# Performance work log

Measured on AMD Instinct MI355X. Metric: run time of the kernel, lower is better.

Reference implementation:

```python
import jax, jax.numpy as jnp
import numpy as np

N_NODES = 50000
NEG_SLOPE = 0.2  # PyG GATConv default leaky_relu slope


def setup_inputs() -> dict:
    key = jax.random.key(0)
    ks = jax.random.split(key, 12)
    N, E, D_IN, H = N_NODES, 1200000, 128, 64
    sd_in = 1.0 / np.sqrt(D_IN)
    sd_h = 1.0 / np.sqrt(H)
    return {
        "x": jax.random.normal(ks[0], (N, D_IN), jnp.float32),
        "src": jax.random.randint(ks[1], (E,), 0, N, jnp.int32),
        "dst": jax.random.randint(ks[2], (E,), 0, N, jnp.int32),
        "W1_src": jax.random.normal(ks[3], (D_IN, H), jnp.float32) * sd_in,
        "W1_dst": jax.random.normal(ks[4], (D_IN, H), jnp.float32) * sd_in,
        "a1_src": jax.random.normal(ks[5], (H,), jnp.float32) * sd_h,
        "a1_dst": jax.random.normal(ks[6], (H,), jnp.float32) * sd_h,
        "b1": jnp.zeros((H,), jnp.float32),
        "W2_src": jax.random.normal(ks[7], (H, H), jnp.float32) * sd_h,
        "W2_dst": jax.random.normal(ks[8], (H, H), jnp.float32) * sd_h,
        "a2_src": jax.random.normal(ks[9], (H,), jnp.float32) * sd_h,
        "a2_dst": jax.random.normal(ks[10], (H,), jnp.float32) * sd_h,
        "b2": jnp.zeros((H,), jnp.float32),
    }


def _gat_layer(x, src, dst, W_src, W_dst, att_src, att_dst, bias):
    N = x.shape[0]
    h_src = x @ W_src            # [N, H] transformed source features
    h_dst = x @ W_dst            # [N, H] transformed destination features
    alpha_src = h_src @ att_src  # [N]
    alpha_dst = h_dst @ att_dst  # [N]
    # edge-wise attention logits (gather), edge j -> i: e = lrelu(a_src[j] + a_dst[i])
    e = jax.nn.leaky_relu(alpha_src[src] + alpha_dst[dst], NEG_SLOPE)  # [E]
    # segment softmax over incoming edges of each destination node
    m = jax.ops.segment_max(e, dst, num_segments=N)          # [N]
    ex = jnp.exp(e - m[dst])                                  # [E]
    denom = jax.ops.segment_sum(ex, dst, num_segments=N)     # [N]
    alpha = ex / denom[dst]                                   # [E]
    # weighted scatter-add aggregation
    msgs = h_src[src] * alpha[:, None]                        # [E, H]
    out = jax.ops.segment_sum(msgs, dst, num_segments=N)     # [N, H]
    return out + bias


def reference(x, src, dst, W1_src, W1_dst, a1_src, a1_dst, b1,
              W2_src, W2_dst, a2_src, a2_dst, b2):
    h = jnp.tanh(_gat_layer(x, src, dst, W1_src, W1_dst, a1_src, a1_dst, b1))
    h = jnp.tanh(_gat_layer(h, src, dst, W2_src, W2_dst, a2_src, a2_dst, b2))
    return h
```

## Files before the change

kernel.cpp:

```cpp
#include <hip/hip_runtime.h>
#include <hip/hip_bf16.h>

#define NEG_SLOPE 0.2f
#define EPB 4096

typedef __attribute__((ext_vector_type(8))) short short8v;
typedef __attribute__((ext_vector_type(4))) float f32x4;

__device__ inline float blo(unsigned u) { return __uint_as_float(u << 16); }
__device__ inline float bhi(unsigned u) { return __uint_as_float(u & 0xffff0000u); }
__device__ inline unsigned short bf16bits(float f) {
    __hip_bfloat16 b = __float2bfloat16(f);
    return *(unsigned short*)&b;
}
__device__ inline unsigned pack2bf(float e, float o) {
    return ((unsigned)bf16bits(o) << 16) | (unsigned)bf16bits(e);
}

__global__ void init_counts(int* __restrict__ bucket_cnt) {
    bucket_cnt[threadIdx.x] = 0;
}

__global__ __launch_bounds__(256) void bucket_hist(const int* __restrict__ dst,
                                                   int* __restrict__ bucket_cnt, int E) {
    __shared__ int lh[256];
    int tid = threadIdx.x;
    lh[tid] = 0;
    __syncthreads();
    for (int e = blockIdx.x * 256 + tid; e < E; e += gridDim.x * 256)
        atomicAdd(&lh[dst[e] >> 8], 1);
    __syncthreads();
    if (lh[tid]) atomicAdd(&bucket_cnt[tid], lh[tid]);
}

__global__ __launch_bounds__(256) void bucket_scan(const int* __restrict__ bucket_cnt,
                                                   int* __restrict__ bucket_base,
                                                   int* __restrict__ bucket_cursor, int NB) {
    __shared__ int tmp[256];
    int tid = threadIdx.x;
    int v = (tid < NB) ? bucket_cnt[tid] : 0;
    tmp[tid] = v;
    __syncthreads();
    for (int off = 1; off < 256; off <<= 1) {
        int t = (tid >= off) ? tmp[tid - off] : 0;
        __syncthreads();
        tmp[tid] += t;
        __syncthreads();
    }
    int excl = tmp[tid] - v;
    bucket_base[tid] = excl;
    bucket_cursor[tid] = excl;
    if (tid == 255) bucket_base[256] = tmp[255];
}

__global__ __launch_bounds__(256) void bucket_scatter(const int* __restrict__ src,
                                                      const int* __restrict__ dst,
                                                      int* __restrict__ bucket_cursor,
                                                      unsigned* __restrict__ ebuf, int E) {
    __shared__ int lhist[256];
    __shared__ int lbase[256];
    int tid = threadIdx.x;
    lhist[tid] = 0;
    __syncthreads();
    int base = blockIdx.x * EPB;
    int bkt[16], rank[16];
    unsigned pack[16];
    #pragma unroll
    for (int i = 0; i < 16; ++i) {
        int e = base + i * 256 + tid;
        bkt[i] = -1;
        if (e < E) {
            int d = dst[e], s = src[e];
            bkt[i]  = d >> 8;
            pack[i] = ((unsigned)(d & 255) << 16) | (unsigned)s;
            rank[i] = atomicAdd(&lhist[bkt[i]], 1);
        }
    }
    __syncthreads();
    int cnt = lhist[tid];
    if (cnt) lbase[tid] = atomicAdd(&bucket_cursor[tid], cnt);
    __syncthreads();
    #pragma unroll
    for (int i = 0; i < 16; ++i)
        if (bkt[i] >= 0) ebuf[lbase[bkt[i]] + rank[i]] = pack[i];
}

__global__ __launch_bounds__(256) void bucket_build(const unsigned* __restrict__ ebuf,
                                                    const int* __restrict__ bucket_base,
                                                    int* __restrict__ row_ptr,
                                                    int* __restrict__ csr_src,
                                                    int N, int E) {
    __shared__ int deg[256];
    __shared__ int cur[256];
    __shared__ int tmp[256];
    int b = blockIdx.x, tid = threadIdx.x;
    int ebase = bucket_base[b], eend = bucket_base[b + 1];
    deg[tid] = 0;
    __syncthreads();
    for (int e = ebase + tid; e < eend; e += 256)
        atomicAdd(&deg[ebuf[e] >> 16], 1);
    __syncthreads();
    int v = deg[tid];
    tmp[tid] = v;
    __syncthreads();
    for (int off = 1; off < 256; off <<= 1) {
        int t = (tid >= off) ? tmp[tid - off] : 0;
        __syncthreads();
        tmp[tid] += t;
        __syncthreads();
    }
    int excl = tmp[tid] - v;
    int node = b * 256 + tid;
    if (node < N) row_ptr[node] = ebase + excl;
    if (b == 0 && tid == 0) row_ptr[N] = E;
    cur[tid] = excl;
    __syncthreads();
    for (int e = ebase + tid; e < eend; e += 256) {
        unsigned pk = ebuf[e];
        int r = atomicAdd(&cur[pk >> 16], 1);
        csr_src[ebase + r] = (int)(pk & 0xFFFFu);
    }
}

template <int K, bool INBF16>
__global__ __launch_bounds__(256) void node_transform_mfma(
    const void* __restrict__ x_,
    const float* __restrict__ W_src,
    const float* __restrict__ a_src,
    const float* __restrict__ W_dst,
    const float* __restrict__ a_dst,
    unsigned* __restrict__ hb_out,
    float* __restrict__ alpha_src,
    float* __restrict__ alpha_dst,
    int N) {
    constexpr int PAD = K + 8;
    __shared__ unsigned short sBt[80 * PAD];
    __shared__ unsigned short sX[64 * PAD];

    int tid = threadIdx.x;
    for (int i = tid; i < 64 * K; i += 256) {
        int k = i >> 6, j = i & 63;
        sBt[j * PAD + k] = bf16bits(W_src[i]);
    }
    for (int i = tid; i < 2 * K; i += 256) {
        int which = (i >= K) ? 1 : 0;
        int k = i - which * K;
        const float* Wr = (which ? W_dst : W_src) + k * 64;
        const float* av = which ? a_dst : a_src;
        float s = 0.f;
        #pragma unroll
        for (int j = 0; j < 64; ++j) s += Wr[j] * av[j];
        sBt[(64 + which) * PAD + k] = bf16bits(s);
    }
    for (int i = tid; i < 14 * K; i += 256) {
        int j = 66 + i / K, k = i % K;
        sBt[j * PAD + k] = 0;
    }
    if constexpr (!INBF16) {
        const float* xb = (const float*)x_;
        for (int idx = tid; idx < 64 * K / 4; idx += 256) {
            int row = (idx * 4) / K, col = (idx * 4) % K;
            int g = blockIdx.x * 64 + row;
            const float4 f = *(const float4*)(xb + (size_t)((g < N) ? g : N - 1) * K + col);
            unsigned short* d = &sX[row * PAD + col];
            d[0] = bf16bits(f.x); d[1] = bf16bits(f.y);
            d[2] = bf16bits(f.z); d[3] = bf16bits(f.w);
        }
    } else {
        const unsigned short* xb = (const unsigned short*)x_;
        for (int idx = tid; idx < 64 * K / 8; idx += 256) {
            int row = (idx * 8) / K, col = (idx * 8) % K;
            int g = blockIdx.x * 64 + row;
            short8v v = *(const short8v*)(xb + (size_t)((g < N) ? g : N - 1) * K + col);
            *(short8v*)&sX[row * PAD + col] = v;
        }
    }
    __syncthreads();

    int wid = tid >> 6, l = tid & 63;
    int rowbase = blockIdx.x * 64 + wid * 16;
    int jcol = l & 15;

    f32x4 acc[5];
    #pragma unroll
    for (int t = 0; t < 5; ++t) acc[t] = (f32x4){0.f, 0.f, 0.f, 0.f};

    const unsigned short* xrow = &sX[(wid * 16 + (l & 15)) * PAD + (l >> 4) * 8];
    #pragma unroll
    for (int kt = 0; kt < K / 32; ++kt) {
        short8v a = *(const short8v*)(xrow + kt * 32);
        int kbase = kt * 32 + (l >> 4) * 8;
        #pragma unroll
        for (int t = 0; t < 5; ++t) {
            short8v b = *(const short8v*)&sBt[(t * 16 + jcol) * PAD + kbase];
            acc[t] = __builtin_amdgcn_mfma_f32_16x16x32_bf16(a, b, acc[t], 0, 0, 0);
        }
    }

    int rbase = rowbase + (l >> 4) * 4;
    #pragma unroll
    for (int t = 0; t < 4; ++t) {
        #pragma unroll
        for (int r = 0; r < 4; ++r) {
            float v = acc[t][r];
            float w = __shfl_xor(v, 1);
            int row = rbase + r;
            if (!(l & 1) && row < N)
                hb_out[(size_t)row * 32 + t * 8 + (jcol >> 1)] = pack2bf(v, w);
        }
    }
    #pragma unroll
    for (int r = 0; r < 4; ++r) {
        int row = rbase + r;
        if (row < N) {
            if (jcol == 0) alpha_src[row] = acc[4][r];
            if (jcol == 1) alpha_dst[row] = acc[4][r];
        }
    }
}

template <bool OUTBF16>
__global__ __launch_bounds__(256) void aggregate(
    const int* __restrict__ row_ptr, const int* __restrict__ csr_src,
    const float* __restrict__ alpha_src, const float* __restrict__ alpha_dst,
    const unsigned* __restrict__ hb,
    const float* __restrict__ bias,
    void* __restrict__ out_,
    int N) {
    int wid = threadIdx.x >> 6, lane = threadIdx.x & 63;
    int node = blockIdx.x * 4 + wid;
    if (node >= N) return;

    int beg = row_ptr[node], end = row_ptr[node + 1];
    float adst = alpha_dst[node];
    int half = lane >> 5, sub = lane & 31;

    float dL = 0.f;
    float aA[4] = {0.f, 0.f, 0.f, 0.f};
    float aB[4] = {0.f, 0.f, 0.f, 0.f};

    for (int c = beg; c < end; c += 64) {
        int cnt = end - c;
        cnt = (cnt < 64) ? cnt : 64;

        int s = 0;
        float p = 0.f;
        if (lane < cnt) {
            s = csr_src[c + lane];
            float t = alpha_src[s] + adst;
            t = (t > 0.f) ? t : NEG_SLOPE * t;
            p = __expf(fminf(t, 60.f));
            dL += p;
        }

        for (int j = 0; j < cnt; j += 16) {
            int   sv[8];
            float pv[8];
            unsigned uv[8];
            #pragma unroll
            for (int i = 0; i < 8; ++i) {
                int e = j + 2 * i + half;
                sv[i] = __shfl(s, e);
                pv[i] = __shfl(p, e);
            }
            #pragma unroll
            for (int i = 0; i < 8; ++i)
                uv[i] = hb[(size_t)sv[i] * 32 + sub];
            #pragma unroll
            for (int i = 0; i < 8; ++i) {
                aA[i & 3] = fmaf(pv[i], blo(uv[i]), aA[i & 3]);
                aB[i & 3] = fmaf(pv[i], bhi(uv[i]), aB[i & 3]);
            }
        }
    }
    float denom = dL;
    #pragma unroll
    for (int off = 32; off; off >>= 1) denom += __shfl_xor(denom, off);

    float accA = (aA[0] + aA[1]) + (aA[2] + aA[3]);
    float accB = (aB[0] + aB[1]) + (aB[2] + aB[3]);
    accA += __shfl_xor(accA, 32);
    accB += __shfl_xor(accB, 32);
    int srcl = lane >> 1;
    float vA = __shfl(accA, srcl);
    float vB = __shfl(accB, srcl);
    float val = (lane & 1) ? vB : vA;
    float r = (denom > 0.f) ? (val / denom) : 0.f;
    float fv = tanhf(r + bias[lane]);

    if constexpr (OUTBF16) {
        float fw = __shfl_xor(fv, 1);
        if (!(lane & 1))
            ((unsigned*)out_)[(size_t)node * 32 + (lane >> 1)] = pack2bf(fv, fw);
    } else {
        ((float*)out_)[(size_t)node * 64 + lane] = fv;
    }
}

extern "C" void kernel_launch(void* const* d_in, const int* in_sizes, int n_in,
                              void* d_out, int out_size, void* d_ws, size_t ws_size,
                              hipStream_t stream) {
    const float* x      = (const float*)d_in[0];
    const int*   src    = (const int*)  d_in[1];
    const int*   dst    = (const int*)  d_in[2];
    const float* W1_src = (const float*)d_in[3];
    const float* W1_dst = (const float*)d_in[4];
    const float* a1_src = (const float*)d_in[5];
    const float* a1_dst = (const float*)d_in[6];
    const float* b1     = (const float*)d_in[7];
    const float* W2_src = (const float*)d_in[8];
    const float* W2_dst = (const float*)d_in[9];
    const float* a2_src = (const float*)d_in[10];
    const float* a2_dst = (const float*)d_in[11];
    const float* b2     = (const float*)d_in[12];
    float* out = (float*)d_out;

    const int N = in_sizes[0] / 128;
    const int E = in_sizes[1];
    const int NB = (N + 255) / 256;

    char* ws = (char*)d_ws;
    size_t off = 0;
    auto alloc = [&](size_t bytes) {
        void* p = ws + off;
        off += (bytes + 255) & ~(size_t)255;
        return p;
    };
    unsigned* hbuf   = (unsigned*)alloc((size_t)N * 32 * 4);
    unsigned* h1buf  = (unsigned*)alloc((size_t)N * 32 * 4);
    float* alpha_src = (float*)alloc((size_t)N * 4);
    float* alpha_dst = (float*)alloc((size_t)N * 4);
    int*   row_ptr   = (int*)  alloc((size_t)(N + 1) * 4);
    int*   csr_src   = (int*)  alloc((size_t)E * 4);
    int*   bucket_cnt    = (int*)alloc(256 * 4);
    int*   bucket_base   = (int*)alloc(257 * 4);
    int*   bucket_cursor = (int*)alloc(256 * 4);
    unsigned* ebuf = (unsigned*)alloc((size_t)E * 4);
    (void)ws_size;

    const int eb3   = (E + EPB - 1) / EPB;
    const int aggb  = (N + 3) / 4;
    const int mfb   = (N + 63) / 64;

    init_counts<<<1, 256, 0, stream>>>(bucket_cnt);
    bucket_hist<<<256, 256, 0, stream>>>(dst, bucket_cnt, E);
    bucket_scan<<<1, 256, 0, stream>>>(bucket_cnt, bucket_base, bucket_cursor, NB);
    bucket_scatter<<<eb3, 256, 0, stream>>>(src, dst, bucket_cursor, ebuf, E);
    bucket_build<<<NB, 256, 0, stream>>>(ebuf, bucket_base, row_ptr, csr_src, N, E);

    node_transform_mfma<128, false><<<mfb, 256, 0, stream>>>(
        x, W1_src, a1_src, W1_dst, a1_dst, hbuf, alpha_src, alpha_dst, N);
    aggregate<true><<<aggb, 256, 0, stream>>>(row_ptr, csr_src, alpha_src, alpha_dst,
                                              hbuf, b1, h1buf, N);

    node_transform_mfma<64, true><<<mfb, 256, 0, stream>>>(
        h1buf, W2_src, a2_src, W2_dst, a2_dst, hbuf, alpha_src, alpha_dst, N);
    aggregate<false><<<aggb, 256, 0, stream>>>(row_ptr, csr_src, alpha_src, alpha_dst,
                                               hbuf, b2, out, N);
}
```

Before: 148.5 us.

## Fuse layer-1 transform with histogram and layer-1 aggregation with layer-2 transform

Layer 1's node transform and the destination histogram now run in one launch, with extra blocks writing per-block partial histograms. Those partials are summed in the scan, so the init kernel and global atomics go away. Layer 1's aggregation is fused with layer 2's MFMA transform: each block aggregates 64 nodes into shared memory and transforms them directly, skipping the global write and re-read of h1. This cuts launches and intermediate memory traffic, but the fused aggregate now runs 16 nodes serially per wave and restages the weights in every block, which may lower parallelism.

```diff
diff --git a/kernel.cpp b/kernel.cpp
--- a/kernel.cpp
+++ b/kernel.cpp
@@ -3,6 +3,7 @@
 
 #define NEG_SLOPE 0.2f
 #define EPB 4096
+#define NHB 64
 
 typedef __attribute__((ext_vector_type(8))) short short8v;
 typedef __attribute__((ext_vector_type(4))) float f32x4;
@@ -17,28 +18,128 @@
     return ((unsigned)bf16bits(o) << 16) | (unsigned)bf16bits(e);
 }
 
-__global__ void init_counts(int* __restrict__ bucket_cnt) {
-    bucket_cnt[threadIdx.x] = 0;
-}
-
-__global__ __launch_bounds__(256) void bucket_hist(const int* __restrict__ dst,
-                                                   int* __restrict__ bucket_cnt, int E) {
+template <int K>
+__device__ inline void stage_sBt(unsigned short* sBt,
+                                 const float* __restrict__ W_src,
+                                 const float* __restrict__ a_src,
+                                 const float* __restrict__ W_dst,
+                                 const float* __restrict__ a_dst, int tid) {
+    constexpr int PAD = K + 8;
+    for (int i = tid; i < 64 * K; i += 256) {
+        int k = i >> 6, j = i & 63;
+        sBt[j * PAD + k] = bf16bits(W_src[i]);
+    }
+    for (int i = tid; i < 2 * K; i += 256) {
+        int which = (i >= K) ? 1 : 0;
+        int k = i - which * K;
+        const float* Wr = (which ? W_dst : W_src) + k * 64;
+        const float* av = which ? a_dst : a_src;
+        float s = 0.f;
+        #pragma unroll
+        for (int j = 0; j < 64; ++j) s += Wr[j] * av[j];
+        sBt[(64 + which) * PAD + k] = bf16bits(s);
+    }
+    for (int i = tid; i < 14 * K; i += 256) {
+        int j = 66 + i / K, k = i % K;
+        sBt[j * PAD + k] = 0;
+    }
+}
+
+template <int K>
+__device__ inline void nt_mfma_body(const unsigned short* sBt,
+                                    const unsigned short* sX,
+                                    int rowblockbase,
+                                    unsigned* __restrict__ hb_out,
+                                    float* __restrict__ alpha_src,
+                                    float* __restrict__ alpha_dst,
+                                    int N, int tid) {
+    constexpr int PAD = K + 8;
+    int wid = tid >> 6, l = tid & 63;
+    int jcol = l & 15;
+
+    f32x4 acc[5];
+    #pragma unroll
+    for (int t = 0; t < 5; ++t) acc[t] = (f32x4){0.f, 0.f, 0.f, 0.f};
+
+    const unsigned short* xrow = &sX[(wid * 16 + (l & 15)) * PAD + (l >> 4) * 8];
+    #pragma unroll
+    for (int kt = 0; kt < K / 32; ++kt) {
+        short8v a = *(const short8v*)(xrow + kt * 32);
+        int kbase = kt * 32 + (l >> 4) * 8;
+        #pragma unroll
+        for (int t = 0; t < 5; ++t) {
+            short8v b = *(const short8v*)&sBt[(t * 16 + jcol) * PAD + kbase];
+            acc[t] = __builtin_amdgcn_mfma_f32_16x16x32_bf16(a, b, acc[t], 0, 0, 0);
+        }
+    }
+
+    int rbase = rowblockbase + wid * 16 + (l >> 4) * 4;
+    #pragma unroll
+    for (int t = 0; t < 4; ++t) {
+        #pragma unroll
+        for (int r = 0; r < 4; ++r) {
+            float v = acc[t][r];
+            float w = __shfl_xor(v, 1);
+            int row = rbase + r;
+            if (!(l & 1) && row < N)
+                hb_out[(size_t)row * 32 + t * 8 + (jcol >> 1)] = pack2bf(v, w);
+        }
+    }
+    #pragma unroll
+    for (int r = 0; r < 4; ++r) {
+        int row = rbase + r;
+        if (row < N) {
+            if (jcol == 0) alpha_src[row] = acc[4][r];
+            if (jcol == 1) alpha_dst[row] = acc[4][r];
+        }
+    }
+}
+
+__global__ __launch_bounds__(256) void fused_nt1_hist(
+    const float* __restrict__ x,
+    const float* __restrict__ W_src, const float* __restrict__ a_src,
+    const float* __restrict__ W_dst, const float* __restrict__ a_dst,
+    unsigned* __restrict__ hb_out, float* __restrict__ alpha_src,
+    float* __restrict__ alpha_dst, int N,
+    const int* __restrict__ dst, int* __restrict__ partials, int E, int ntb) {
+    constexpr int K = 128, PAD = K + 8;
+    __shared__ unsigned short sBt[80 * PAD];
+    __shared__ unsigned short sX[64 * PAD];
     __shared__ int lh[256];
     int tid = threadIdx.x;
-    lh[tid] = 0;
-    __syncthreads();
-    for (int e = blockIdx.x * 256 + tid; e < E; e += gridDim.x * 256)
-        atomicAdd(&lh[dst[e] >> 8], 1);
-    __syncthreads();
-    if (lh[tid]) atomicAdd(&bucket_cnt[tid], lh[tid]);
-}
-
-__global__ __launch_bounds__(256) void bucket_scan(const int* __restrict__ bucket_cnt,
+
+    if ((int)blockIdx.x >= ntb) {
+        int bh = blockIdx.x - ntb;
+        lh[tid] = 0;
+        __syncthreads();
+        for (int e = bh * 256 + tid; e < E; e += NHB * 256)
+            atomicAdd(&lh[dst[e] >> 8], 1);
+        __syncthreads();
+        partials[bh * 256 + tid] = lh[tid];
+        return;
+    }
+
+    stage_sBt<K>(sBt, W_src, a_src, W_dst, a_dst, tid);
+    for (int idx = tid; idx < 64 * K / 4; idx += 256) {
+        int row = (idx * 4) / K, col = (idx * 4) % K;
+        int g = blockIdx.x * 64 + row;
+        const float4 f = *(const float4*)(x + (size_t)((g < N) ? g : N - 1) * K + col);
+        unsigned short* d = &sX[row * PAD + col];
+        d[0] = bf16bits(f.x); d[1] = bf16bits(f.y);
+        d[2] = bf16bits(f.z); d[3] = bf16bits(f.w);
+    }
+    __syncthreads();
+    nt_mfma_body<K>(sBt, sX, blockIdx.x * 64, hb_out, alpha_src, alpha_dst, N, tid);
+}
+
+__global__ __launch_bounds__(256) void bucket_scan(const int* __restrict__ partials,
                                                    int* __restrict__ bucket_base,
-                                                   int* __restrict__ bucket_cursor, int NB) {
+                                                   int* __restrict__ bucket_cursor) {
     __shared__ int tmp[256];
     int tid = threadIdx.x;
-    int v = (tid < NB) ? bucket_cnt[tid] : 0;
+    int v = 0;
+    #pragma unroll 8
+    for (int b = 0; b < NHB; ++b) v += partials[b * 256 + tid];
     tmp[tid] = v;
     __syncthreads();
     for (int off = 1; off < 256; off <<= 1) {
@@ -122,115 +223,12 @@
     }
 }
 
-template <int K, bool INBF16>
-__global__ __launch_bounds__(256) void node_transform_mfma(
-    const void* __restrict__ x_,
-    const float* __restrict__ W_src,
-    const float* __restrict__ a_src,
-    const float* __restrict__ W_dst,
-    const float* __restrict__ a_dst,
-    unsigned* __restrict__ hb_out,
-    float* __restrict__ alpha_src,
-    float* __restrict__ alpha_dst,
-    int N) {
-    constexpr int PAD = K + 8;
-    __shared__ unsigned short sBt[80 * PAD];
-    __shared__ unsigned short sX[64 * PAD];
-
-    int tid = threadIdx.x;
-    for (int i = tid; i < 64 * K; i += 256) {
-        int k = i >> 6, j = i & 63;
-        sBt[j * PAD + k] = bf16bits(W_src[i]);
-    }
-    for (int i = tid; i < 2 * K; i += 256) {
-        int which = (i >= K) ? 1 : 0;
-        int k = i - which * K;
-        const float* Wr = (which ? W_dst : W_src) + k * 64;
-        const float* av = which ? a_dst : a_src;
-        float s = 0.f;
-        #pragma unroll
-        for (int j = 0; j < 64; ++j) s += Wr[j] * av[j];
-        sBt[(64 + which) * PAD + k] = bf16bits(s);
-    }
-    for (int i = tid; i < 14 * K; i += 256) {
-        int j = 66 + i / K, k = i % K;
-        sBt[j * PAD + k] = 0;
-    }
-    if constexpr (!INBF16) {
-        const float* xb = (const float*)x_;
-        for (int idx = tid; idx < 64 * K / 4; idx += 256) {
-            int row = (idx * 4) / K, col = (idx * 4) % K;
-            int g = blockIdx.x * 64 + row;
-            const float4 f = *(const float4*)(xb + (size_t)((g < N) ? g : N - 1) * K + col);
-            unsigned short* d = &sX[row * PAD + col];
-            d[0] = bf16bits(f.x); d[1] = bf16bits(f.y);
-            d[2] = bf16bits(f.z); d[3] = bf16bits(f.w);
-        }
-    } else {
-        const unsigned short* xb = (const unsigned short*)x_;
-        for (int idx = tid; idx < 64 * K / 8; idx += 256) {
-            int row = (idx * 8) / K, col = (idx * 8) % K;
-            int g = blockIdx.x * 64 + row;
-            short8v v = *(const short8v*)(xb + (size_t)((g < N) ? g : N - 1) * K + col);
-            *(short8v*)&sX[row * PAD + col] = v;
-        }
-    }
-    __syncthreads();
-
-    int wid = tid >> 6, l = tid & 63;
-    int rowbase = blockIdx.x * 64 + wid * 16;
-    int jcol = l & 15;
-
-    f32x4 acc[5];
-    #pragma unroll
-    for (int t = 0; t < 5; ++t) acc[t] = (f32x4){0.f, 0.f, 0.f, 0.f};
-
-    const unsigned short* xrow = &sX[(wid * 16 + (l & 15)) * PAD + (l >> 4) * 8];
-    #pragma unroll
-    for (int kt = 0; kt < K / 32; ++kt) {
-        short8v a = *(const short8v*)(xrow + kt * 32);
-        int kbase = kt * 32 + (l >> 4) * 8;
-        #pragma unroll
-        for (int t = 0; t < 5; ++t) {
-            short8v b = *(const short8v*)&sBt[(t * 16 + jcol) * PAD + kbase];
-            acc[t] = __builtin_amdgcn_mfma_f32_16x16x32_bf16(a, b, acc[t], 0, 0, 0);
-        }
-    }
-
-    int rbase = rowbase + (l >> 4) * 4;
-    #pragma unroll
-    for (int t = 0; t < 4; ++t) {
-        #pragma unroll
-        for (int r = 0; r < 4; ++r) {
-            float v = acc[t][r];
-            float w = __shfl_xor(v, 1);
-            int row = rbase + r;
-            if (!(l & 1) && row < N)
-                hb_out[(size_t)row * 32 + t * 8 + (jcol >> 1)] = pack2bf(v, w);
-        }
-    }
-    #pragma unroll
-    for (int r = 0; r < 4; ++r) {
-        int row = rbase + r;
-        if (row < N) {
-            if (jcol == 0) alpha_src[row] = acc[4][r];
-            if (jcol == 1) alpha_dst[row] = acc[4][r];
-        }
-    }
-}
-
-template <bool OUTBF16>
-__global__ __launch_bounds__(256) void aggregate(
-    const int* __restrict__ row_ptr, const int* __restrict__ csr_src,
-    const float* __restrict__ alpha_src, const float* __restrict__ alpha_dst,
-    const unsigned* __restrict__ hb,
-    const float* __restrict__ bias,
-    void* __restrict__ out_,
-    int N) {
-    int wid = threadIdx.x >> 6, lane = threadIdx.x & 63;
-    int node = blockIdx.x * 4 + wid;
-    if (node >= N) return;
-
+__device__ inline float agg_node(int node, const int* __restrict__ row_ptr,
+                                 const int* __restrict__ csr_src,
+                                 const float* __restrict__ alpha_src,
+                                 const float* __restrict__ alpha_dst,
+                                 const unsigned* __restrict__ hb,
+                                 float blane, int lane) {
     int beg = row_ptr[node], end = row_ptr[node + 1];
     float adst = alpha_dst[node];
     int half = lane >> 5, sub = lane & 31;
@@ -286,15 +284,52 @@
     float vB = __shfl(accB, srcl);
     float val = (lane & 1) ? vB : vA;
     float r = (denom > 0.f) ? (val / denom) : 0.f;
-    float fv = tanhf(r + bias[lane]);
-
-    if constexpr (OUTBF16) {
-        float fw = __shfl_xor(fv, 1);
-        if (!(lane & 1))
-            ((unsigned*)out_)[(size_t)node * 32 + (lane >> 1)] = pack2bf(fv, fw);
-    } else {
-        ((float*)out_)[(size_t)node * 64 + lane] = fv;
-    }
+    return tanhf(r + blane);
+}
+
+__global__ __launch_bounds__(256) void fused_agg_nt(
+    const int* __restrict__ row_ptr, const int* __restrict__ csr_src,
+    const float* __restrict__ alpha_src1, const float* __restrict__ alpha_dst1,
+    const unsigned* __restrict__ hb1,
+    const float* __restrict__ bias1,
+    const float* __restrict__ W_src, const float* __restrict__ a_src,
+    const float* __restrict__ W_dst, const float* __restrict__ a_dst,
+    unsigned* __restrict__ hb2, float* __restrict__ alpha_src2,
+    float* __restrict__ alpha_dst2, int N) {
+    constexpr int K = 64, PAD = K + 8;
+    __shared__ unsigned short sBt[80 * PAD];
+    __shared__ unsigned short sX[64 * PAD];
+    int tid = threadIdx.x;
+
+    stage_sBt<K>(sBt, W_src, a_src, W_dst, a_dst, tid);
+
+    int wid = tid >> 6, lane = tid & 63;
+    int blockbase = blockIdx.x * 64;
+    float blane = bias1[lane];
+
+    for (int i = 0; i < 16; ++i) {
+        int node = blockbase + wid * 16 + i;
+        float fv = 0.f;
+        if (node < N)
+            fv = agg_node(node, row_ptr, csr_src, alpha_src1, alpha_dst1, hb1,
+                          blane, lane);
+        sX[(wid * 16 + i) * PAD + lane] = bf16bits(fv);
+    }
+    __syncthreads();
+    nt_mfma_body<K>(sBt, sX, blockbase, hb2, alpha_src2, alpha_dst2, N, tid);
+}
+
+__global__ __launch_bounds__(256) void aggregate_out(
+    const int* __restrict__ row_ptr, const int* __restrict__ csr_src,
+    const float* __restrict__ alpha_src, const float* __restrict__ alpha_dst,
+    const unsigned* __restrict__ hb, const float* __restrict__ bias,
+    float* __restrict__ out, int N) {
+    int wid = threadIdx.x >> 6, lane = threadIdx.x & 63;
+    int node = blockIdx.x * 4 + wid;
+    if (node >= N) return;
+    float fv = agg_node(node, row_ptr, csr_src, alpha_src, alpha_dst, hb,
+                        bias[lane], lane);
+    out[(size_t)node * 64 + lane] = fv;
 }
 
 extern "C" void kernel_launch(void* const* d_in, const int* in_sizes, int n_in,
@@ -326,35 +361,33 @@
         off += (bytes + 255) & ~(size_t)255;
         return p;
     };
-    unsigned* hbuf   = (unsigned*)alloc((size_t)N * 32 * 4);
-    unsigned* h1buf  = (unsigned*)alloc((size_t)N * 32 * 4);
-    float* alpha_src = (float*)alloc((size_t)N * 4);
-    float* alpha_dst = (float*)alloc((size_t)N * 4);
-    int*   row_ptr   = (int*)  alloc((size_t)(N + 1) * 4);
-    int*   csr_src   = (int*)  alloc((size_t)E * 4);
-    int*   bucket_cnt    = (int*)alloc(256 * 4);
+    unsigned* hbuf1   = (unsigned*)alloc((size_t)N * 32 * 4);
+    unsigned* hbuf2   = (unsigned*)alloc((size_t)N * 32 * 4);
+    float* alpha_s1   = (float*)alloc((size_t)N * 4);
+    float* alpha_d1   = (float*)alloc((size_t)N * 4);
+    float* alpha_s2   = (float*)alloc((size_t)N * 4);
+    float* alpha_d2   = (float*)alloc((size_t)N * 4);
+    int*   row_ptr    = (int*)  alloc((size_t)(N + 1) * 4);
+    int*   csr_src    = (int*)  alloc((size_t)E * 4);
+    int*   partials   = (int*)  alloc(NHB * 256 * 4);
     int*   bucket_base   = (int*)alloc(257 * 4);
     int*   bucket_cursor = (int*)alloc(256 * 4);
-    unsigned* ebuf = (unsigned*)alloc((size_t)E * 4);
-    (void)ws_size;
-
-    const int eb3   = (E + EPB - 1) / EPB;
-    const int aggb  = (N + 3) / 4;
-    const int mfb   = (N + 63) / 64;
-
-    init_counts<<<1, 256, 0, stream>>>(bucket_cnt);
-    bucket_hist<<<256, 256, 0, stream>>>(dst, bucket_cnt, E);
-    bucket_scan<<<1, 256, 0, stream>>>(bucket_cnt, bucket_base, bucket_cursor, NB);
+    unsigned* ebuf    = (unsigned*)alloc((size_t)E * 4);
+    (void)ws_size; (void)NB;
+
+    const int eb3  = (E + EPB - 1) / EPB;
+    const int aggb = (N + 3) / 4;
+    const int ntb  = (N + 63) / 64;
+
+    fused_nt1_hist<<<ntb + NHB, 256, 0, stream>>>(
+        x, W1_src, a1_src, W1_dst, a1_dst, hbuf1, alpha_s1, alpha_d1, N,
+        dst, partials, E, ntb);
+    bucket_scan<<<1, 256, 0, stream>>>(partials, bucket_base, bucket_cursor);
     bucket_scatter<<<eb3, 256, 0, stream>>>(src, dst, bucket_cursor, ebuf, E);
     bucket_build<<<NB, 256, 0, stream>>>(ebuf, bucket_base, row_ptr, csr_src, N, E);
-
-    node_transform_mfma<128, false><<<mfb, 256, 0, stream>>>(
-        x, W1_src, a1_src, W1_dst, a1_dst, hbuf, alpha_src, alpha_dst, N);
-    aggregate<true><<<aggb, 256, 0, stream>>>(row_ptr, csr_src, alpha_src, alpha_dst,
-                                              hbuf, b1, h1buf, N);
-
-    node_transform_mfma<64, true><<<mfb, 256, 0, stream>>>(
-        h1buf, W2_src, a2_src, W2_dst, a2_dst, hbuf, alpha_src, alpha_dst, N);
-    aggregate<false><<<aggb, 256, 0, stream>>>(row_ptr, csr_src, alpha_src, alpha_dst,
-                                               hbuf, b2, out, N);
-}
+    fused_agg_nt<<<ntb, 256, 0, stream>>>(
+        row_ptr, csr_src, alpha_s1, alpha_d1, hbuf1, b1,
+        W2_src, a2_src, W2_dst, a2_dst, hbuf2, alpha_s2, alpha_d2, N);
+    aggregate_out<<<aggb, 256, 0, stream>>>(
+        row_ptr, csr_src, alpha_s2, alpha_d2, hbuf2, b2, out, N);
+}
```

After: 154.8 us. 1.04x slower.

## Precompute bf16 weight tiles once and load node features directly to registers

Applied to the files above, without the earlier changes.

The bf16 transposed weight matrices (plus the folded attention vectors) are now built once in a prep kernel, not redundantly in every node-transform block. The node transform drops its shared-memory staging and reads x rows and weight rows straight from global memory into MFMA operands. The histogram now writes per-block partials that the scan reduces, which removes the init kernel and the global atomics. The cost is uncoalesced-ish global weight reads per wave, served from cache, plus extra buffers for the second layer.

```diff
diff --git a/kernel.cpp b/kernel.cpp
--- a/kernel.cpp
+++ b/kernel.cpp
@@ -3,6 +3,7 @@
 
 #define NEG_SLOPE 0.2f
 #define EPB 4096
+#define NHB 64
 
 typedef __attribute__((ext_vector_type(8))) short short8v;
 typedef __attribute__((ext_vector_type(4))) float f32x4;
@@ -17,28 +18,60 @@
     return ((unsigned)bf16bits(o) << 16) | (unsigned)bf16bits(e);
 }
 
-__global__ void init_counts(int* __restrict__ bucket_cnt) {
-    bucket_cnt[threadIdx.x] = 0;
-}
-
-__global__ __launch_bounds__(256) void bucket_hist(const int* __restrict__ dst,
-                                                   int* __restrict__ bucket_cnt, int E) {
+template <int K>
+__device__ inline void build_wt(unsigned short* __restrict__ Wt,
+                                const float* __restrict__ W_src,
+                                const float* __restrict__ a_src,
+                                const float* __restrict__ W_dst,
+                                const float* __restrict__ a_dst, int tid) {
+    for (int i = tid; i < 64 * K; i += 256) {
+        int k = i >> 6, j = i & 63;
+        Wt[j * K + k] = bf16bits(W_src[i]);
+    }
+    for (int i = tid; i < 2 * K; i += 256) {
+        int which = (i >= K) ? 1 : 0;
+        int k = i - which * K;
+        const float* Wr = (which ? W_dst : W_src) + k * 64;
+        const float* av = which ? a_dst : a_src;
+        float s = 0.f;
+        #pragma unroll
+        for (int j = 0; j < 64; ++j) s += Wr[j] * av[j];
+        Wt[(64 + which) * K + k] = bf16bits(s);
+    }
+    for (int i = tid; i < 14 * K; i += 256) Wt[66 * K + i] = 0;
+}
+
+__global__ __launch_bounds__(256) void prep(
+    const int* __restrict__ dst, int* __restrict__ partials, int E,
+    const float* __restrict__ W1_src, const float* __restrict__ a1_src,
+    const float* __restrict__ W1_dst, const float* __restrict__ a1_dst,
+    const float* __restrict__ W2_src, const float* __restrict__ a2_src,
+    const float* __restrict__ W2_dst, const float* __restrict__ a2_dst,
+    unsigned short* __restrict__ Wt1, unsigned short* __restrict__ Wt2) {
     __shared__ int lh[256];
-    int tid = threadIdx.x;
-    lh[tid] = 0;
-    __syncthreads();
-    for (int e = blockIdx.x * 256 + tid; e < E; e += gridDim.x * 256)
-        atomicAdd(&lh[dst[e] >> 8], 1);
-    __syncthreads();
-    if (lh[tid]) atomicAdd(&bucket_cnt[tid], lh[tid]);
-}
-
-__global__ __launch_bounds__(256) void bucket_scan(const int* __restrict__ bucket_cnt,
+    int tid = threadIdx.x, b = blockIdx.x;
+    if (b < NHB) {
+        lh[tid] = 0;
+        __syncthreads();
+        for (int e = b * 256 + tid; e < E; e += NHB * 256)
+            atomicAdd(&lh[dst[e] >> 8], 1);
+        __syncthreads();
+        partials[b * 256 + tid] = lh[tid];
+    } else if (b == NHB) {
+        build_wt<128>(Wt1, W1_src, a1_src, W1_dst, a1_dst, tid);
+    } else {
+        build_wt<64>(Wt2, W2_src, a2_src, W2_dst, a2_dst, tid);
+    }
+}
+
+__global__ __launch_bounds__(256) void bucket_scan(const int* __restrict__ partials,
                                                    int* __restrict__ bucket_base,
-                                                   int* __restrict__ bucket_cursor, int NB) {
+                                                   int* __restrict__ bucket_cursor) {
     __shared__ int tmp[256];
     int tid = threadIdx.x;
-    int v = (tid < NB) ? bucket_cnt[tid] : 0;
+    int v = 0;
+    #pragma unroll 8
+    for (int b = 0; b < NHB; ++b) v += partials[b * 256 + tid];
     tmp[tid] = v;
     __syncthreads();
     for (int off = 1; off < 256; off <<= 1) {
@@ -123,76 +156,43 @@
 }
 
 template <int K, bool INBF16>
-__global__ __launch_bounds__(256) void node_transform_mfma(
+__global__ __launch_bounds__(256) void nt_reg(
     const void* __restrict__ x_,
-    const float* __restrict__ W_src,
-    const float* __restrict__ a_src,
-    const float* __restrict__ W_dst,
-    const float* __restrict__ a_dst,
+    const unsigned short* __restrict__ Wt,
     unsigned* __restrict__ hb_out,
-    float* __restrict__ alpha_src,
-    float* __restrict__ alpha_dst,
-    int N) {
-    constexpr int PAD = K + 8;
-    __shared__ unsigned short sBt[80 * PAD];
-    __shared__ unsigned short sX[64 * PAD];
-
+    float* __restrict__ alpha_src, float* __restrict__ alpha_dst, int N) {
     int tid = threadIdx.x;
-    for (int i = tid; i < 64 * K; i += 256) {
-        int k = i >> 6, j = i & 63;
-        sBt[j * PAD + k] = bf16bits(W_src[i]);
-    }
-    for (int i = tid; i < 2 * K; i += 256) {
-        int which = (i >= K) ? 1 : 0;
-        int k = i - which * K;
-        const float* Wr = (which ? W_dst : W_src) + k * 64;
-        const float* av = which ? a_dst : a_src;
-        float s = 0.f;
-        #pragma unroll
-        for (int j = 0; j < 64; ++j) s += Wr[j] * av[j];
-        sBt[(64 + which) * PAD + k] = bf16bits(s);
-    }
-    for (int i = tid; i < 14 * K; i += 256) {
-        int j = 66 + i / K, k = i % K;
-        sBt[j * PAD + k] = 0;
-    }
-    if constexpr (!INBF16) {
-        const float* xb = (const float*)x_;
-        for (int idx = tid; idx < 64 * K / 4; idx += 256) {
-            int row = (idx * 4) / K, col = (idx * 4) % K;
-            int g = blockIdx.x * 64 + row;
-            const float4 f = *(const float4*)(xb + (size_t)((g < N) ? g : N - 1) * K + col);
-            unsigned short* d = &sX[row * PAD + col];
-            d[0] = bf16bits(f.x); d[1] = bf16bits(f.y);
-            d[2] = bf16bits(f.z); d[3] = bf16bits(f.w);
-        }
-    } else {
-        const unsigned short* xb = (const unsigned short*)x_;
-        for (int idx = tid; idx < 64 * K / 8; idx += 256) {
-            int row = (idx * 8) / K, col = (idx * 8) % K;
-            int g = blockIdx.x * 64 + row;
-            short8v v = *(const short8v*)(xb + (size_t)((g < N) ? g : N - 1) * K + col);
-            *(short8v*)&sX[row * PAD + col] = v;
-        }
-    }
-    __syncthreads();
-
     int wid = tid >> 6, l = tid & 63;
-    int rowbase = blockIdx.x * 64 + wid * 16;
-    int jcol = l & 15;
+    int rowbase = (blockIdx.x * 4 + wid) * 16;
+    if (rowbase >= N) return;
+    int jcol = l & 15, kg = (l >> 4) * 8;
+
+    int r = rowbase + jcol;
+    if (r >= N) r = N - 1;
+    const float*          xr32 = (const float*)x_ + (size_t)r * K + kg;
+    const unsigned short* xr16 = (const unsigned short*)x_ + (size_t)r * K + kg;
 
     f32x4 acc[5];
     #pragma unroll
     for (int t = 0; t < 5; ++t) acc[t] = (f32x4){0.f, 0.f, 0.f, 0.f};
 
-    const unsigned short* xrow = &sX[(wid * 16 + (l & 15)) * PAD + (l >> 4) * 8];
     #pragma unroll
     for (int kt = 0; kt < K / 32; ++kt) {
-        short8v a = *(const short8v*)(xrow + kt * 32);
-        int kbase = kt * 32 + (l >> 4) * 8;
+        short8v a;
+        if constexpr (INBF16) {
+            a = *(const short8v*)(xr16 + kt * 32);
+        } else {
+            float4 xa = *(const float4*)(xr32 + kt * 32);
+            float4 xb = *(const float4*)(xr32 + kt * 32 + 4);
+            a[0] = (short)bf16bits(xa.x); a[1] = (short)bf16bits(xa.y);
+            a[2] = (short)bf16bits(xa.z); a[3] = (short)bf16bits(xa.w);
+            a[4] = (short)bf16bits(xb.x); a[5] = (short)bf16bits(xb.y);
+            a[6] = (short)bf16bits(xb.z); a[7] = (short)bf16bits(xb.w);
+        }
+        int kbase = kt * 32 + kg;
         #pragma unroll
         for (int t = 0; t < 5; ++t) {
-            short8v b = *(const short8v*)&sBt[(t * 16 + jcol) * PAD + kbase];
+            short8v b = *(const short8v*)&Wt[(t * 16 + jcol) * K + kbase];
             acc[t] = __builtin_amdgcn_mfma_f32_16x16x32_bf16(a, b, acc[t], 0, 0, 0);
         }
     }
@@ -201,20 +201,20 @@
     #pragma unroll
     for (int t = 0; t < 4; ++t) {
         #pragma unroll
-        for (int r = 0; r < 4; ++r) {
-            float v = acc[t][r];
+        for (int rr = 0; rr < 4; ++rr) {
+            float v = acc[t][rr];
             float w = __shfl_xor(v, 1);
-            int row = rbase + r;
+            int row = rbase + rr;
             if (!(l & 1) && row < N)
                 hb_out[(size_t)row * 32 + t * 8 + (jcol >> 1)] = pack2bf(v, w);
         }
     }
     #pragma unroll
-    for (int r = 0; r < 4; ++r) {
-        int row = rbase + r;
+    for (int rr = 0; rr < 4; ++rr) {
+        int row = rbase + rr;
         if (row < N) {
-            if (jcol == 0) alpha_src[row] = acc[4][r];
-            if (jcol == 1) alpha_dst[row] = acc[4][r];
+            if (jcol == 0) alpha_src[row] = acc[4][rr];
+            if (jcol == 1) alpha_dst[row] = acc[4][rr];
         }
     }
 }
@@ -326,35 +326,38 @@
         off += (bytes + 255) & ~(size_t)255;
         return p;
     };
-    unsigned* hbuf   = (unsigned*)alloc((size_t)N * 32 * 4);
+    unsigned* hbuf1  = (unsigned*)alloc((size_t)N * 32 * 4);
     unsigned* h1buf  = (unsigned*)alloc((size_t)N * 32 * 4);
-    float* alpha_src = (float*)alloc((size_t)N * 4);
-    float* alpha_dst = (float*)alloc((size_t)N * 4);
+    unsigned* hbuf2  = (unsigned*)alloc((size_t)N * 32 * 4);
+    float* alpha_s1  = (float*)alloc((size_t)N * 4);
+    float* alpha_d1  = (float*)alloc((size_t)N * 4);
+    float* alpha_s2  = (float*)alloc((size_t)N * 4);
+    float* alpha_d2  = (float*)alloc((size_t)N * 4);
     int*   row_ptr   = (int*)  alloc((size_t)(N + 1) * 4);
     int*   csr_src   = (int*)  alloc((size_t)E * 4);
-    int*   bucket_cnt    = (int*)alloc(256 * 4);
+    int*   partials  = (int*)  alloc(NHB * 256 * 4);
     int*   bucket_base   = (int*)alloc(257 * 4);
     int*   bucket_cursor = (int*)alloc(256 * 4);
-    unsigned* ebuf = (unsigned*)alloc((size_t)E * 4);
+    unsigned short* Wt1 = (unsigned short*)alloc(80 * 128 * 2);
+    unsigned short* Wt2 = (unsigned short*)alloc(80 * 64 * 2);
+    unsigned* ebuf   = (unsigned*)alloc((size_t)E * 4);
     (void)ws_size;
 
-    const int eb3   = (E + EPB - 1) / EPB;
-    const int aggb  = (N + 3) / 4;
-    const int mfb   = (N + 63) / 64;
-
-    init_counts<<<1, 256, 0, stream>>>(bucket_cnt);
-    bucket_hist<<<256, 256, 0, stream>>>(dst, bucket_cnt, E);
-    bucket_scan<<<1, 256, 0, stream>>>(bucket_cnt, bucket_base, bucket_cursor, NB);
+    const int eb3  = (E + EPB - 1) / EPB;
+    const int nwb  = (N + 3) / 4;
+    const int ntb  = (N + 63) / 64;
+
+    prep<<<NHB + 2, 256, 0, stream>>>(dst, partials, E,
+                                      W1_src, a1_src, W1_dst, a1_dst,
+                                      W2_src, a2_src, W2_dst, a2_dst, Wt1, Wt2);
+    bucket_scan<<<1, 256, 0, stream>>>(partials, bucket_base, bucket_cursor);
     bucket_scatter<<<eb3, 256, 0, stream>>>(src, dst, bucket_cursor, ebuf, E);
     bucket_build<<<NB, 256, 0, stream>>>(ebuf, bucket_base, row_ptr, csr_src, N, E);
 
-    node_transform_mfma<128, false><<<mfb, 256, 0, stream>>>(
-        x, W1_src, a1_src, W1_dst, a1_dst, hbuf, alpha_src, alpha_dst, N);
-    aggregate<true><<<aggb, 256, 0, stream>>>(row_ptr, csr_src, alpha_src, alpha_dst,
-                                              hbuf, b1, h1buf, N);
-
-    node_transform_mfma<64, true><<<mfb, 256, 0, stream>>>(
-        h1buf, W2_src, a2_src, W2_dst, a2_dst, hbuf, alpha_src, alpha_dst, N);
-    aggregate<false><<<aggb, 256, 0, stream>>>(row_ptr, csr_src, alpha_src, alpha_dst,
-                                               hbuf, b2, out, N);
-}
+    nt_reg<128, false><<<ntb, 256, 0, stream>>>(x, Wt1, hbuf1, alpha_s1, alpha_d1, N);
+    aggregate<true><<<nwb, 256, 0, stream>>>(row_ptr, csr_src, alpha_s1, alpha_d1,
+                                             hbuf1, b1, h1buf, N);
+    nt_reg<64, true><<<ntb, 256, 0, stream>>>(h1buf, Wt2, hbuf2, alpha_s2, alpha_d2, N);
+    aggregate<false><<<nwb, 256, 0, stream>>>(row_ptr, csr_src, alpha_s2, alpha_d2,
+                                              hbuf2, b2, out, N);
+}
```

After: 144.4 us. 1.03x faster.
